# Kernel optimization log

Measured on AMD Instinct MI355X. Metric: run time of the kernel, lower is better.

Reference implementation:

```python
import jax, jax.numpy as jnp
import numpy as np


def gcn_conv(x, edge_index, W, b):
    # PyG GCNConv: h = x @ W; add self-loops; symmetric D^-1/2 (A+I) D^-1/2 aggregation; + bias
    n = x.shape[0]
    h = x @ W  # [N, out]
    loop = jnp.arange(n, dtype=edge_index.dtype)
    src = jnp.concatenate([edge_index[0], loop])  # message sources
    dst = jnp.concatenate([edge_index[1], loop])  # message targets
    ones = jnp.ones(dst.shape[0], dtype=h.dtype)
    deg = jax.ops.segment_sum(ones, dst, num_segments=n)  # in-degree incl. self-loop
    dinv = jnp.where(deg > 0, jax.lax.rsqrt(deg), 0.0)
    norm = dinv[src] * dinv[dst]  # [E+N]
    msg = h[src] * norm[:, None]  # gather + scale
    out = jax.ops.segment_sum(msg, dst, num_segments=n)  # scatter-add
    return out + b


def setup_inputs() -> dict:
    key = jax.random.key(0)
    ks = jax.random.split(key, 6)
    N, E, D = 100000, 600000, 128
    x = jax.random.normal(ks[0], (N, D), dtype=jnp.float32)
    edge_index = jax.random.randint(ks[1], (2, E), 0, N, dtype=jnp.int64)
    s = 1.0 / np.sqrt(D)
    W1 = jax.random.normal(ks[2], (D, D), dtype=jnp.float32) * s
    b1 = jnp.zeros((D,), dtype=jnp.float32)
    W2 = jax.random.normal(ks[3], (2 * D, D), dtype=jnp.float32) * (1.0 / np.sqrt(2 * D))
    b2 = jnp.zeros((D,), dtype=jnp.float32)
    Wout = jax.random.normal(ks[4], (D, 1), dtype=jnp.float32) * s
    bout = jnp.zeros((1,), dtype=jnp.float32)
    return {"x": x, "edge_index": edge_index, "W1": W1, "b1": b1,
            "W2": W2, "b2": b2, "Wout": Wout, "bout": bout}


def reference(x, edge_index, W1, b1, W2, b2, Wout, bout):
    y = gcn_conv(x, edge_index, W1, b1)          # [N, D]
    y = jnp.concatenate([x, y], axis=-1)          # [N, 2D]
    y = jax.nn.leaky_relu(y, negative_slope=0.01)
    z = gcn_conv(y, edge_index, W2, b2)           # [N, D]
    z = jax.nn.leaky_relu(z, negative_slope=0.01)
    return z @ Wout + bout                        # [N, 1]
```

## Files before the change

kernel.cpp:

```cpp
#include <hip/hip_runtime.h>

#define DIM 128
#define CAP 48

typedef _Float16 half8 __attribute__((ext_vector_type(8)));
typedef float f32x4 __attribute__((ext_vector_type(4)));

__device__ __forceinline__ float lrelu(float v) { return v > 0.f ? v : 0.01f * v; }


__global__ __launch_bounds__(256) void k_zero(int* __restrict__ cursor, int n) {
    int i = blockIdx.x * 256 + threadIdx.x;
    if (i < n) cursor[i] = 0;
}

__global__ __launch_bounds__(256) void k_fill(const int* __restrict__ src,
                                              const int* __restrict__ dst,
                                              int* __restrict__ cursor,
                                              int* __restrict__ srcs, int e) {
    int i = blockIdx.x * 256 + threadIdx.x;
    if (i >= e) return;
    int d = dst[i];
    int p = atomicAdd(&cursor[d], 1);
    if (p < CAP) srcs[(size_t)d * CAP + p] = src[i];
}

__global__ __launch_bounds__(256) void k_dinv(const int* __restrict__ cursor,
                                              float* __restrict__ dinv, int n) {
    int i = blockIdx.x * 256 + threadIdx.x;
    if (i < n) dinv[i] = rsqrtf((float)cursor[i] + 1.0f);
}

__global__ __launch_bounds__(256) void k_pack(const float* __restrict__ W,
                                              _Float16* __restrict__ Wp, int kdim) {
    int tid = blockIdx.x * 256 + threadIdx.x;
    if (tid >= kdim * 128) return;
    int jj = tid & 7;
    int frag = tid >> 3;
    int l = frag & 63;
    int cb = (frag >> 6) & 7;
    int kb = frag >> 9;
    int k = kb * 32 + ((l >> 4) << 3) + jj;
    int nn = cb * 16 + (l & 15);
    Wp[tid] = (_Float16)W[(size_t)k * DIM + nn];
}

__global__ __launch_bounds__(256, 2) void k_mm1(
    const float* __restrict__ x, const _Float16* __restrict__ Wp1,
    const _Float16* __restrict__ Wp2, const float* __restrict__ dinv,
    _Float16* __restrict__ hs, _Float16* __restrict__ P, int n) {
    __shared__ _Float16 As[8 * 4 * 64 * 8];
    const int tid = threadIdx.x;
    const int w = tid >> 6, l = tid & 63;
    const int row0 = blockIdx.x * 128;
    {
        const int c8 = (tid & 15) * 8;
        const int kb = c8 >> 5, sub = (c8 & 31) >> 3;
#pragma unroll
        for (int it = 0; it < 8; ++it) {
            int r = it * 16 + (tid >> 4);
            int grow = row0 + r;
            float4 v0 = make_float4(0.f, 0.f, 0.f, 0.f), v1 = v0;
            if (grow < n) {
                const float4* xr = (const float4*)&x[(size_t)grow * DIM + c8];
                v0 = xr[0]; v1 = xr[1];
            }
            half8 o;
            o[0] = (_Float16)v0.x; o[1] = (_Float16)v0.y;
            o[2] = (_Float16)v0.z; o[3] = (_Float16)v0.w;
            o[4] = (_Float16)v1.x; o[5] = (_Float16)v1.y;
            o[6] = (_Float16)v1.z; o[7] = (_Float16)v1.w;
            int rb = r >> 4;
            int li = sub * 16 + (r & 15);
            int p = li ^ (kb << 2);
            *(half8*)&As[(((rb << 2) + kb) * 64 + p) * 8] = o;
        }
    }
    __syncthreads();

    f32x4 ah[4][4], ap[4][4];
#pragma unroll
    for (int i = 0; i < 4; ++i)
#pragma unroll
        for (int j = 0; j < 4; ++j) {
            f32x4 z = {0.f, 0.f, 0.f, 0.f};
            ah[i][j] = z; ap[i][j] = z;
        }

    const int rwb = (w >> 1) * 4, cwb = (w & 1) * 4;
#pragma unroll
    for (int kb = 0; kb < 4; ++kb) {
        half8 a[4], al[4], b[4];
#pragma unroll
        for (int i = 0; i < 4; ++i)
            a[i] = *(const half8*)&As[((((rwb + i) << 2) + kb) * 64 + (l ^ (kb << 2))) * 8];
#pragma unroll
        for (int i = 0; i < 4; ++i)
#pragma unroll
            for (int e = 0; e < 8; ++e) {
                _Float16 t = a[i][e];
                al[i][e] = (t > (_Float16)0.f) ? t : t * (_Float16)0.01f;
            }
#pragma unroll
        for (int j = 0; j < 4; ++j)
            b[j] = *(const half8*)&Wp1[((kb * 8 + cwb + j) * 64 + l) * 8];
#pragma unroll
        for (int i = 0; i < 4; ++i)
#pragma unroll
            for (int j = 0; j < 4; ++j)
                ah[i][j] = __builtin_amdgcn_mfma_f32_16x16x32_f16(a[i], b[j], ah[i][j], 0, 0, 0);
#pragma unroll
        for (int j = 0; j < 4; ++j)
            b[j] = *(const half8*)&Wp2[((kb * 8 + cwb + j) * 64 + l) * 8];
#pragma unroll
        for (int i = 0; i < 4; ++i)
#pragma unroll
            for (int j = 0; j < 4; ++j)
                ap[i][j] = __builtin_amdgcn_mfma_f32_16x16x32_f16(al[i], b[j], ap[i][j], 0, 0, 0);
    }
#pragma unroll
    for (int i = 0; i < 4; ++i) {
        int rbase = (rwb + i) * 16 + ((l >> 4) << 2);
#pragma unroll
        for (int reg = 0; reg < 4; ++reg) {
            int grow = row0 + rbase + reg;
            if (grow < n) {
                float d = dinv[grow];
#pragma unroll
                for (int j = 0; j < 4; ++j) {
                    int col = (cwb + j) * 16 + (l & 15);
                    hs[(size_t)grow * DIM + col] = (_Float16)(ah[i][j][reg] * d);
                }
            }
        }
    }
    _Float16* pl = P + ((size_t)(blockIdx.x * 4 + w) * 64 + l) * 64;
#pragma unroll
    for (int c = 0; c < 8; ++c) {
        int q0 = 2 * c, q1 = 2 * c + 1;
        half8 o;
#pragma unroll
        for (int e = 0; e < 4; ++e) {
            o[e]     = (_Float16)ap[q0 >> 2][q0 & 3][e];
            o[4 + e] = (_Float16)ap[q1 >> 2][q1 & 3][e];
        }
        *(half8*)&pl[c * 8] = o;
    }
}

__global__ __launch_bounds__(256) void k_mm2(
    const _Float16* __restrict__ A2, const _Float16* __restrict__ Wp2,
    const _Float16* __restrict__ P, const float* __restrict__ dinv,
    _Float16* __restrict__ hs2, int n) {
    __shared__ _Float16 As[8 * 4 * 64 * 8];
    const int tid = threadIdx.x;
    const int w = tid >> 6, l = tid & 63;
    const int row0 = blockIdx.x * 128;
    const _Float16* at = A2 + (size_t)blockIdx.x * 16384;
#pragma unroll
    for (int it = 0; it < 8; ++it) {
        int idx = it * 256 + tid;
        *(half8*)&As[idx * 8] = *(const half8*)&at[(size_t)idx * 8];
    }
    __syncthreads();

    f32x4 acc[4][4];
#pragma unroll
    for (int i = 0; i < 4; ++i)
#pragma unroll
        for (int j = 0; j < 4; ++j) { f32x4 z = {0.f, 0.f, 0.f, 0.f}; acc[i][j] = z; }

    const int rwb = (w >> 1) * 4, cwb = (w & 1) * 4;
#pragma unroll
    for (int kb = 0; kb < 4; ++kb) {
        half8 a[4], b[4];
#pragma unroll
        for (int i = 0; i < 4; ++i)
            a[i] = *(const half8*)&As[((((rwb + i) << 2) + kb) * 64 + l) * 8];
#pragma unroll
        for (int j = 0; j < 4; ++j)
            b[j] = *(const half8*)&Wp2[(((kb + 4) * 8 + cwb + j) * 64 + l) * 8];
#pragma unroll
        for (int i = 0; i < 4; ++i)
#pragma unroll
            for (int j = 0; j < 4; ++j)
                acc[i][j] = __builtin_amdgcn_mfma_f32_16x16x32_f16(a[i], b[j], acc[i][j], 0, 0, 0);
    }
    const _Float16* pl = P + ((size_t)(blockIdx.x * 4 + w) * 64 + l) * 64;
#pragma unroll
    for (int c = 0; c < 8; ++c) {
        half8 pv = *(const half8*)&pl[c * 8];
        int q0 = 2 * c, q1 = 2 * c + 1;
#pragma unroll
        for (int e = 0; e < 4; ++e) {
            acc[q0 >> 2][q0 & 3][e] += (float)pv[e];
            acc[q1 >> 2][q1 & 3][e] += (float)pv[4 + e];
        }
    }
#pragma unroll
    for (int i = 0; i < 4; ++i) {
        int rbase = (rwb + i) * 16 + ((l >> 4) << 2);
#pragma unroll
        for (int reg = 0; reg < 4; ++reg) {
            int grow = row0 + rbase + reg;
            if (grow < n) {
                float d = dinv[grow];
#pragma unroll
                for (int j = 0; j < 4; ++j) {
                    int col = (cwb + j) * 16 + (l & 15);
                    hs2[(size_t)grow * DIM + col] = (_Float16)(acc[i][j][reg] * d);
                }
            }
        }
    }
}

__global__ __launch_bounds__(256) void k_gather1(
    const _Float16* __restrict__ hs, const int* __restrict__ cursor,
    const int* __restrict__ srcs, const float* __restrict__ dinv,
    const float* __restrict__ b1, _Float16* __restrict__ A2, int n) {
    const int node = blockIdx.x * 16 + (threadIdx.x >> 4);
    const int g = threadIdx.x & 15;
    if (node >= n) return;
    int cnt = cursor[node];
    if (cnt > CAP) cnt = CAP;
    const int* sl = &srcs[(size_t)node * CAP];
    half8 h = *(const half8*)&hs[(size_t)node * DIM + g * 8];
    float acc[8];
#pragma unroll
    for (int e = 0; e < 8; ++e) acc[e] = (float)h[e];
    for (int base = 0; base < cnt; base += 16) {
        int m = cnt - base;
        if (m > 16) m = 16;
        int sid = (g < m) ? sl[base + g] : 0;
#pragma unroll 4
        for (int j = 0; j < m; ++j) {
            int s = __shfl(sid, j, 16);
            half8 v = *(const half8*)&hs[(size_t)s * DIM + g * 8];
#pragma unroll
            for (int e = 0; e < 8; ++e) acc[e] += (float)v[e];
        }
    }
    const float d = dinv[node];
    const float4 bb0 = *(const float4*)&b1[g * 8];
    const float4 bb1 = *(const float4*)&b1[g * 8 + 4];
    half8 o;
    o[0] = (_Float16)lrelu(fmaf(acc[0], d, bb0.x));
    o[1] = (_Float16)lrelu(fmaf(acc[1], d, bb0.y));
    o[2] = (_Float16)lrelu(fmaf(acc[2], d, bb0.z));
    o[3] = (_Float16)lrelu(fmaf(acc[3], d, bb0.w));
    o[4] = (_Float16)lrelu(fmaf(acc[4], d, bb1.x));
    o[5] = (_Float16)lrelu(fmaf(acc[5], d, bb1.y));
    o[6] = (_Float16)lrelu(fmaf(acc[6], d, bb1.z));
    o[7] = (_Float16)lrelu(fmaf(acc[7], d, bb1.w));
    int tile = node >> 7, rb = (node >> 4) & 7, rr = node & 15;
    int kb = g >> 2, sub = g & 3;
    *(half8*)&A2[(size_t)tile * 16384 + ((((rb << 2) + kb) * 64) + sub * 16 + rr) * 8] = o;
}

__global__ __launch_bounds__(256) void k_gather2(
    const _Float16* __restrict__ hs2, const int* __restrict__ cursor,
    const int* __restrict__ srcs, const float* __restrict__ dinv,
    const float* __restrict__ b2, const float* __restrict__ wout,
    const float* __restrict__ bout, float* __restrict__ out, int n) {
    const int node = blockIdx.x * 16 + (threadIdx.x >> 4);
    const int g = threadIdx.x & 15;
    if (node >= n) return;
    int cnt = cursor[node];
    if (cnt > CAP) cnt = CAP;
    const int* sl = &srcs[(size_t)node * CAP];
    half8 h = *(const half8*)&hs2[(size_t)node * DIM + g * 8];
    float acc[8];
#pragma unroll
    for (int e = 0; e < 8; ++e) acc[e] = (float)h[e];
    for (int base = 0; base < cnt; base += 16) {
        int m = cnt - base;
        if (m > 16) m = 16;
        int sid = (g < m) ? sl[base + g] : 0;
#pragma unroll 4
        for (int j = 0; j < m; ++j) {
            int s = __shfl(sid, j, 16);
            half8 v = *(const half8*)&hs2[(size_t)s * DIM + g * 8];
#pragma unroll
            for (int e = 0; e < 8; ++e) acc[e] += (float)v[e];
        }
    }
    const float d = dinv[node];
    const float4 bb0 = *(const float4*)&b2[g * 8];
    const float4 bb1 = *(const float4*)&b2[g * 8 + 4];
    const float4 wv0 = *(const float4*)&wout[g * 8];
    const float4 wv1 = *(const float4*)&wout[g * 8 + 4];
    float s = lrelu(fmaf(acc[0], d, bb0.x)) * wv0.x + lrelu(fmaf(acc[1], d, bb0.y)) * wv0.y +
              lrelu(fmaf(acc[2], d, bb0.z)) * wv0.z + lrelu(fmaf(acc[3], d, bb0.w)) * wv0.w +
              lrelu(fmaf(acc[4], d, bb1.x)) * wv1.x + lrelu(fmaf(acc[5], d, bb1.y)) * wv1.y +
              lrelu(fmaf(acc[6], d, bb1.z)) * wv1.z + lrelu(fmaf(acc[7], d, bb1.w)) * wv1.w;
#pragma unroll
    for (int off = 8; off > 0; off >>= 1) s += __shfl_down(s, off, 16);
    if (g == 0) out[node] = s + bout[0];
}

extern "C" void kernel_launch(void* const* d_in, const int* in_sizes, int n_in,
                              void* d_out, int out_size, void* d_ws, size_t ws_size,
                              hipStream_t stream) {
    const float* x    = (const float*)d_in[0];
    const int*   ei   = (const int*)d_in[1];
    const float* W1   = (const float*)d_in[2];
    const float* b1   = (const float*)d_in[3];
    const float* W2   = (const float*)d_in[4];
    const float* b2   = (const float*)d_in[5];
    const float* Wout = (const float*)d_in[6];
    const float* bout = (const float*)d_in[7];
    float* out = (float*)d_out;

    const int N = in_sizes[0] / DIM;
    const int E = in_sizes[1] / 2;
    const int* src = ei;
    const int* dst = ei + E;

    const int gb = (N + 127) / 128;
    const size_t tileH = (size_t)gb * 16384;

    size_t Na = ((size_t)N + 63) & ~(size_t)63;
    int* cursor   = (int*)d_ws;
    float* dinv   = (float*)(cursor + Na);
    int* srcs     = (int*)(dinv + Na);
    _Float16* Wp1 = (_Float16*)(srcs + (size_t)N * CAP);
    _Float16* Wp2 = Wp1 + 128 * 128;
    _Float16* hsb = Wp2 + 256 * 128;
    _Float16* Pb  = hsb + tileH;
    _Float16* A2b = Pb + tileH;

    const int nb = (N + 255) / 256;
    const int eb = (E + 255) / 256;
    const int ab = (N + 15) / 16;

    k_zero<<<nb, 256, 0, stream>>>(cursor, N);
    k_fill<<<eb, 256, 0, stream>>>(src, dst, cursor, srcs, E);
    k_dinv<<<nb, 256, 0, stream>>>(cursor, dinv, N);
    k_pack<<<(128 * 128 + 255) / 256, 256, 0, stream>>>(W1, Wp1, 128);
    k_pack<<<(256 * 128 + 255) / 256, 256, 0, stream>>>(W2, Wp2, 256);

    k_mm1<<<gb, 256, 0, stream>>>(x, Wp1, Wp2, dinv, hsb, Pb, N);
    k_gather1<<<ab, 256, 0, stream>>>(hsb, cursor, srcs, dinv, b1, A2b, N);
    k_mm2<<<gb, 256, 0, stream>>>(A2b, Wp2, Pb, dinv, hsb, N);
    k_gather2<<<ab, 256, 0, stream>>>(hsb, cursor, srcs, dinv, b2, Wout, bout, out, N);
}
```

Before: 246.5 us.

## Fuse layer-1 gather into second GEMM and merge preprocessing kernels

Folds the first-layer neighbour aggregation into the second GEMM kernel, so the aggregated tile goes straight into shared memory and the A2 intermediate buffer is no longer written to or read from global memory. Edge fill and both weight-packing passes are merged into one kernel, and the zeroing kernel becomes a memset. The degree-normalisation array is gone; rsqrt is recomputed from the cursor counts wherever it is needed. GEMM tiles shrink to 64 rows, and the first GEMM loads A fragments directly from global memory with no LDS staging. The second-layer output is written in place over the P buffer, which saves workspace but depends on each block reading its own P tile before overwriting it.

Result: faster. 234.3 us (-4.9%).

```diff
diff --git a/kernel.cpp b/kernel.cpp
--- a/kernel.cpp
+++ b/kernel.cpp
@@ -8,271 +8,211 @@
 
 __device__ __forceinline__ float lrelu(float v) { return v > 0.f ? v : 0.01f * v; }
 
-
-__global__ __launch_bounds__(256) void k_zero(int* __restrict__ cursor, int n) {
-    int i = blockIdx.x * 256 + threadIdx.x;
-    if (i < n) cursor[i] = 0;
-}
-
-__global__ __launch_bounds__(256) void k_fill(const int* __restrict__ src,
-                                              const int* __restrict__ dst,
-                                              int* __restrict__ cursor,
-                                              int* __restrict__ srcs, int e) {
-    int i = blockIdx.x * 256 + threadIdx.x;
-    if (i >= e) return;
-    int d = dst[i];
-    int p = atomicAdd(&cursor[d], 1);
-    if (p < CAP) srcs[(size_t)d * CAP + p] = src[i];
-}
-
-__global__ __launch_bounds__(256) void k_dinv(const int* __restrict__ cursor,
-                                              float* __restrict__ dinv, int n) {
-    int i = blockIdx.x * 256 + threadIdx.x;
-    if (i < n) dinv[i] = rsqrtf((float)cursor[i] + 1.0f);
-}
-
-__global__ __launch_bounds__(256) void k_pack(const float* __restrict__ W,
-                                              _Float16* __restrict__ Wp, int kdim) {
-    int tid = blockIdx.x * 256 + threadIdx.x;
-    if (tid >= kdim * 128) return;
-    int jj = tid & 7;
-    int frag = tid >> 3;
+__global__ __launch_bounds__(256) void k_prep(
+    const int* __restrict__ src, const int* __restrict__ dst,
+    int* __restrict__ cursor, int* __restrict__ srcs, int e, int eb,
+    const float* __restrict__ W1, _Float16* __restrict__ Wp1,
+    const float* __restrict__ W2, _Float16* __restrict__ Wp2) {
+    int b = blockIdx.x;
+    if (b < eb) {
+        int i = b * 256 + threadIdx.x;
+        if (i < e) {
+            int d = dst[i];
+            int p = atomicAdd(&cursor[d], 1);
+            if (p < CAP) srcs[(size_t)d * CAP + p] = src[i];
+        }
+        return;
+    }
+    b -= eb;
+    const float* W;
+    _Float16* Wp;
+    int tid2;
+    if (b < 64) { W = W1; Wp = Wp1; tid2 = b * 256 + threadIdx.x; }
+    else        { W = W2; Wp = Wp2; tid2 = (b - 64) * 256 + threadIdx.x; }
+    int jj = tid2 & 7;
+    int frag = tid2 >> 3;
     int l = frag & 63;
     int cb = (frag >> 6) & 7;
     int kb = frag >> 9;
     int k = kb * 32 + ((l >> 4) << 3) + jj;
     int nn = cb * 16 + (l & 15);
-    Wp[tid] = (_Float16)W[(size_t)k * DIM + nn];
+    Wp[tid2] = (_Float16)W[(size_t)k * DIM + nn];
 }
 
 __global__ __launch_bounds__(256, 2) void k_mm1(
     const float* __restrict__ x, const _Float16* __restrict__ Wp1,
-    const _Float16* __restrict__ Wp2, const float* __restrict__ dinv,
+    const _Float16* __restrict__ Wp2, const int* __restrict__ cursor,
     _Float16* __restrict__ hs, _Float16* __restrict__ P, int n) {
-    __shared__ _Float16 As[8 * 4 * 64 * 8];
     const int tid = threadIdx.x;
     const int w = tid >> 6, l = tid & 63;
-    const int row0 = blockIdx.x * 128;
-    {
-        const int c8 = (tid & 15) * 8;
-        const int kb = c8 >> 5, sub = (c8 & 31) >> 3;
-#pragma unroll
-        for (int it = 0; it < 8; ++it) {
-            int r = it * 16 + (tid >> 4);
-            int grow = row0 + r;
-            float4 v0 = make_float4(0.f, 0.f, 0.f, 0.f), v1 = v0;
-            if (grow < n) {
-                const float4* xr = (const float4*)&x[(size_t)grow * DIM + c8];
-                v0 = xr[0]; v1 = xr[1];
-            }
-            half8 o;
-            o[0] = (_Float16)v0.x; o[1] = (_Float16)v0.y;
-            o[2] = (_Float16)v0.z; o[3] = (_Float16)v0.w;
-            o[4] = (_Float16)v1.x; o[5] = (_Float16)v1.y;
-            o[6] = (_Float16)v1.z; o[7] = (_Float16)v1.w;
-            int rb = r >> 4;
-            int li = sub * 16 + (r & 15);
-            int p = li ^ (kb << 2);
-            *(half8*)&As[(((rb << 2) + kb) * 64 + p) * 8] = o;
-        }
-    }
-    __syncthreads();
-
-    f32x4 ah[4][4], ap[4][4];
-#pragma unroll
-    for (int i = 0; i < 4; ++i)
-#pragma unroll
-        for (int j = 0; j < 4; ++j) {
-            f32x4 z = {0.f, 0.f, 0.f, 0.f};
-            ah[i][j] = z; ap[i][j] = z;
-        }
-
-    const int rwb = (w >> 1) * 4, cwb = (w & 1) * 4;
+    const int row0 = blockIdx.x * 64;
+    const int arow = row0 + w * 16 + (l & 15);
+    const int kq = (l >> 4) << 3;
+    const bool ok = arow < n;
+    const float* xr = &x[(size_t)arow * DIM + kq];
+
+    f32x4 ah[8], ap[8];
+#pragma unroll
+    for (int cb = 0; cb < 8; ++cb) {
+        f32x4 z = {0.f, 0.f, 0.f, 0.f};
+        ah[cb] = z; ap[cb] = z;
+    }
+
 #pragma unroll
     for (int kb = 0; kb < 4; ++kb) {
-        half8 a[4], al[4], b[4];
-#pragma unroll
-        for (int i = 0; i < 4; ++i)
-            a[i] = *(const half8*)&As[((((rwb + i) << 2) + kb) * 64 + (l ^ (kb << 2))) * 8];
-#pragma unroll
-        for (int i = 0; i < 4; ++i)
-#pragma unroll
-            for (int e = 0; e < 8; ++e) {
-                _Float16 t = a[i][e];
-                al[i][e] = (t > (_Float16)0.f) ? t : t * (_Float16)0.01f;
-            }
-#pragma unroll
-        for (int j = 0; j < 4; ++j)
-            b[j] = *(const half8*)&Wp1[((kb * 8 + cwb + j) * 64 + l) * 8];
-#pragma unroll
-        for (int i = 0; i < 4; ++i)
-#pragma unroll
-            for (int j = 0; j < 4; ++j)
-                ah[i][j] = __builtin_amdgcn_mfma_f32_16x16x32_f16(a[i], b[j], ah[i][j], 0, 0, 0);
-#pragma unroll
-        for (int j = 0; j < 4; ++j)
-            b[j] = *(const half8*)&Wp2[((kb * 8 + cwb + j) * 64 + l) * 8];
-#pragma unroll
-        for (int i = 0; i < 4; ++i)
-#pragma unroll
-            for (int j = 0; j < 4; ++j)
-                ap[i][j] = __builtin_amdgcn_mfma_f32_16x16x32_f16(al[i], b[j], ap[i][j], 0, 0, 0);
-    }
-#pragma unroll
-    for (int i = 0; i < 4; ++i) {
-        int rbase = (rwb + i) * 16 + ((l >> 4) << 2);
-#pragma unroll
-        for (int reg = 0; reg < 4; ++reg) {
-            int grow = row0 + rbase + reg;
-            if (grow < n) {
-                float d = dinv[grow];
-#pragma unroll
-                for (int j = 0; j < 4; ++j) {
-                    int col = (cwb + j) * 16 + (l & 15);
-                    hs[(size_t)grow * DIM + col] = (_Float16)(ah[i][j][reg] * d);
+        float4 v0 = make_float4(0.f, 0.f, 0.f, 0.f), v1 = v0;
+        if (ok) {
+            v0 = *(const float4*)&xr[kb * 32];
+            v1 = *(const float4*)&xr[kb * 32 + 4];
+        }
+        half8 a, al;
+        a[0] = (_Float16)v0.x; a[1] = (_Float16)v0.y;
+        a[2] = (_Float16)v0.z; a[3] = (_Float16)v0.w;
+        a[4] = (_Float16)v1.x; a[5] = (_Float16)v1.y;
+        a[6] = (_Float16)v1.z; a[7] = (_Float16)v1.w;
+#pragma unroll
+        for (int e = 0; e < 8; ++e) {
+            _Float16 t = a[e];
+            al[e] = (t > (_Float16)0.f) ? t : t * (_Float16)0.01f;
+        }
+#pragma unroll
+        for (int cb = 0; cb < 8; ++cb) {
+            half8 bf = *(const half8*)&Wp1[((kb * 8 + cb) * 64 + l) * 8];
+            ah[cb] = __builtin_amdgcn_mfma_f32_16x16x32_f16(a, bf, ah[cb], 0, 0, 0);
+        }
+#pragma unroll
+        for (int cb = 0; cb < 8; ++cb) {
+            half8 bf = *(const half8*)&Wp2[((kb * 8 + cb) * 64 + l) * 8];
+            ap[cb] = __builtin_amdgcn_mfma_f32_16x16x32_f16(al, bf, ap[cb], 0, 0, 0);
+        }
+    }
+    const int orow0 = row0 + w * 16 + ((l >> 4) << 2);
+    const int oc = l & 15;
+#pragma unroll
+    for (int reg = 0; reg < 4; ++reg) {
+        int grow = orow0 + reg;
+        if (grow < n) {
+            float d = rsqrtf((float)cursor[grow] + 1.0f);
+#pragma unroll
+            for (int cb = 0; cb < 8; ++cb)
+                hs[(size_t)grow * DIM + cb * 16 + oc] = (_Float16)(ah[cb][reg] * d);
+        }
+    }
+    _Float16* pl = P + ((size_t)(blockIdx.x * 4 + w) * 64 + l) * 32;
+#pragma unroll
+    for (int c = 0; c < 4; ++c) {
+        half8 o;
+#pragma unroll
+        for (int e = 0; e < 4; ++e) {
+            o[e]     = (_Float16)ap[2 * c][e];
+            o[4 + e] = (_Float16)ap[2 * c + 1][e];
+        }
+        *(half8*)&pl[c * 8] = o;
+    }
+}
+
+__global__ __launch_bounds__(256, 2) void k_mm2g(
+    const _Float16* __restrict__ hs, const int* __restrict__ cursor,
+    const int* __restrict__ srcs, const float* __restrict__ b1,
+    const _Float16* __restrict__ Wp2, const _Float16* __restrict__ P,
+    _Float16* __restrict__ hs2, int n) {
+    __shared__ _Float16 Af[16 * 64 * 8];
+    const int tid = threadIdx.x;
+    const int w = tid >> 6, l = tid & 63;
+    const int row0 = blockIdx.x * 64;
+
+    f32x4 acc[8];
+    const _Float16* pl = P + ((size_t)(blockIdx.x * 4 + w) * 64 + l) * 32;
+#pragma unroll
+    for (int c = 0; c < 4; ++c) {
+        half8 pv = *(const half8*)&pl[c * 8];
+#pragma unroll
+        for (int e = 0; e < 4; ++e) {
+            acc[2 * c][e]     = (float)pv[e];
+            acc[2 * c + 1][e] = (float)pv[4 + e];
+        }
+    }
+
+    const int g = tid & 15;
+#pragma unroll
+    for (int it = 0; it < 4; ++it) {
+        int node = row0 + it * 16 + (tid >> 4);
+        half8 o = 0;
+        if (node < n) {
+            int rawc = cursor[node];
+            float d = rsqrtf((float)rawc + 1.0f);
+            int cnt = rawc > CAP ? CAP : rawc;
+            const int* sl = &srcs[(size_t)node * CAP];
+            half8 h = *(const half8*)&hs[(size_t)node * DIM + g * 8];
+            float a[8];
+#pragma unroll
+            for (int e = 0; e < 8; ++e) a[e] = (float)h[e];
+            for (int base = 0; base < cnt; base += 16) {
+                int m = cnt - base;
+                if (m > 16) m = 16;
+                int sid = (g < m) ? sl[base + g] : 0;
+#pragma unroll 4
+                for (int j = 0; j < m; ++j) {
+                    int s = __shfl(sid, j, 16);
+                    half8 v = *(const half8*)&hs[(size_t)s * DIM + g * 8];
+#pragma unroll
+                    for (int e = 0; e < 8; ++e) a[e] += (float)v[e];
                 }
             }
-        }
-    }
-    _Float16* pl = P + ((size_t)(blockIdx.x * 4 + w) * 64 + l) * 64;
-#pragma unroll
-    for (int c = 0; c < 8; ++c) {
-        int q0 = 2 * c, q1 = 2 * c + 1;
-        half8 o;
-#pragma unroll
-        for (int e = 0; e < 4; ++e) {
-            o[e]     = (_Float16)ap[q0 >> 2][q0 & 3][e];
-            o[4 + e] = (_Float16)ap[q1 >> 2][q1 & 3][e];
-        }
-        *(half8*)&pl[c * 8] = o;
-    }
-}
-
-__global__ __launch_bounds__(256) void k_mm2(
-    const _Float16* __restrict__ A2, const _Float16* __restrict__ Wp2,
-    const _Float16* __restrict__ P, const float* __restrict__ dinv,
-    _Float16* __restrict__ hs2, int n) {
-    __shared__ _Float16 As[8 * 4 * 64 * 8];
-    const int tid = threadIdx.x;
-    const int w = tid >> 6, l = tid & 63;
-    const int row0 = blockIdx.x * 128;
-    const _Float16* at = A2 + (size_t)blockIdx.x * 16384;
-#pragma unroll
-    for (int it = 0; it < 8; ++it) {
-        int idx = it * 256 + tid;
-        *(half8*)&As[idx * 8] = *(const half8*)&at[(size_t)idx * 8];
+            const float4 bb0 = *(const float4*)&b1[g * 8];
+            const float4 bb1 = *(const float4*)&b1[g * 8 + 4];
+            o[0] = (_Float16)lrelu(fmaf(a[0], d, bb0.x));
+            o[1] = (_Float16)lrelu(fmaf(a[1], d, bb0.y));
+            o[2] = (_Float16)lrelu(fmaf(a[2], d, bb0.z));
+            o[3] = (_Float16)lrelu(fmaf(a[3], d, bb0.w));
+            o[4] = (_Float16)lrelu(fmaf(a[4], d, bb1.x));
+            o[5] = (_Float16)lrelu(fmaf(a[5], d, bb1.y));
+            o[6] = (_Float16)lrelu(fmaf(a[6], d, bb1.z));
+            o[7] = (_Float16)lrelu(fmaf(a[7], d, bb1.w));
+        }
+        *(half8*)&Af[(((it * 4 + (g >> 2)) * 64) + (g & 3) * 16 + (tid >> 4)) * 8] = o;
     }
     __syncthreads();
 
-    f32x4 acc[4][4];
-#pragma unroll
-    for (int i = 0; i < 4; ++i)
-#pragma unroll
-        for (int j = 0; j < 4; ++j) { f32x4 z = {0.f, 0.f, 0.f, 0.f}; acc[i][j] = z; }
-
-    const int rwb = (w >> 1) * 4, cwb = (w & 1) * 4;
 #pragma unroll
     for (int kb = 0; kb < 4; ++kb) {
-        half8 a[4], b[4];
-#pragma unroll
-        for (int i = 0; i < 4; ++i)
-            a[i] = *(const half8*)&As[((((rwb + i) << 2) + kb) * 64 + l) * 8];
-#pragma unroll
-        for (int j = 0; j < 4; ++j)
-            b[j] = *(const half8*)&Wp2[(((kb + 4) * 8 + cwb + j) * 64 + l) * 8];
-#pragma unroll
-        for (int i = 0; i < 4; ++i)
-#pragma unroll
-            for (int j = 0; j < 4; ++j)
-                acc[i][j] = __builtin_amdgcn_mfma_f32_16x16x32_f16(a[i], b[j], acc[i][j], 0, 0, 0);
-    }
-    const _Float16* pl = P + ((size_t)(blockIdx.x * 4 + w) * 64 + l) * 64;
-#pragma unroll
-    for (int c = 0; c < 8; ++c) {
-        half8 pv = *(const half8*)&pl[c * 8];
-        int q0 = 2 * c, q1 = 2 * c + 1;
-#pragma unroll
-        for (int e = 0; e < 4; ++e) {
-            acc[q0 >> 2][q0 & 3][e] += (float)pv[e];
-            acc[q1 >> 2][q1 & 3][e] += (float)pv[4 + e];
-        }
-    }
-#pragma unroll
-    for (int i = 0; i < 4; ++i) {
-        int rbase = (rwb + i) * 16 + ((l >> 4) << 2);
-#pragma unroll
-        for (int reg = 0; reg < 4; ++reg) {
-            int grow = row0 + rbase + reg;
-            if (grow < n) {
-                float d = dinv[grow];
-#pragma unroll
-                for (int j = 0; j < 4; ++j) {
-                    int col = (cwb + j) * 16 + (l & 15);
-                    hs2[(size_t)grow * DIM + col] = (_Float16)(acc[i][j][reg] * d);
-                }
-            }
-        }
-    }
-}
-
-__global__ __launch_bounds__(256) void k_gather1(
-    const _Float16* __restrict__ hs, const int* __restrict__ cursor,
-    const int* __restrict__ srcs, const float* __restrict__ dinv,
-    const float* __restrict__ b1, _Float16* __restrict__ A2, int n) {
+        half8 a = *(const half8*)&Af[((w * 4 + kb) * 64 + l) * 8];
+#pragma unroll
+        for (int cb = 0; cb < 8; ++cb) {
+            half8 bf = *(const half8*)&Wp2[(((kb + 4) * 8 + cb) * 64 + l) * 8];
+            acc[cb] = __builtin_amdgcn_mfma_f32_16x16x32_f16(a, bf, acc[cb], 0, 0, 0);
+        }
+    }
+    const int orow0 = row0 + w * 16 + ((l >> 4) << 2);
+    const int oc = l & 15;
+#pragma unroll
+    for (int reg = 0; reg < 4; ++reg) {
+        int grow = orow0 + reg;
+        if (grow < n) {
+            float d = rsqrtf((float)cursor[grow] + 1.0f);
+#pragma unroll
+            for (int cb = 0; cb < 8; ++cb)
+                hs2[(size_t)grow * DIM + cb * 16 + oc] = (_Float16)(acc[cb][reg] * d);
+        }
+    }
+}
+
+__global__ __launch_bounds__(256) void k_gather2(
+    const _Float16* __restrict__ hs2, const int* __restrict__ cursor,
+    const int* __restrict__ srcs, const float* __restrict__ b2,
+    const float* __restrict__ wout, const float* __restrict__ bout,
+    float* __restrict__ out, int n) {
     const int node = blockIdx.x * 16 + (threadIdx.x >> 4);
     const int g = threadIdx.x & 15;
     if (node >= n) return;
-    int cnt = cursor[node];
-    if (cnt > CAP) cnt = CAP;
-    const int* sl = &srcs[(size_t)node * CAP];
-    half8 h = *(const half8*)&hs[(size_t)node * DIM + g * 8];
-    float acc[8];
-#pragma unroll
-    for (int e = 0; e < 8; ++e) acc[e] = (float)h[e];
-    for (int base = 0; base < cnt; base += 16) {
-        int m = cnt - base;
-        if (m > 16) m = 16;
-        int sid = (g < m) ? sl[base + g] : 0;
-#pragma unroll 4
-        for (int j = 0; j < m; ++j) {
-            int s = __shfl(sid, j, 16);
-            half8 v = *(const half8*)&hs[(size_t)s * DIM + g * 8];
-#pragma unroll
-            for (int e = 0; e < 8; ++e) acc[e] += (float)v[e];
-        }
-    }
-    const float d = dinv[node];
-    const float4 bb0 = *(const float4*)&b1[g * 8];
-    const float4 bb1 = *(const float4*)&b1[g * 8 + 4];
-    half8 o;
-    o[0] = (_Float16)lrelu(fmaf(acc[0], d, bb0.x));
-    o[1] = (_Float16)lrelu(fmaf(acc[1], d, bb0.y));
-    o[2] = (_Float16)lrelu(fmaf(acc[2], d, bb0.z));
-    o[3] = (_Float16)lrelu(fmaf(acc[3], d, bb0.w));
-    o[4] = (_Float16)lrelu(fmaf(acc[4], d, bb1.x));
-    o[5] = (_Float16)lrelu(fmaf(acc[5], d, bb1.y));
-    o[6] = (_Float16)lrelu(fmaf(acc[6], d, bb1.z));
-    o[7] = (_Float16)lrelu(fmaf(acc[7], d, bb1.w));
-    int tile = node >> 7, rb = (node >> 4) & 7, rr = node & 15;
-    int kb = g >> 2, sub = g & 3;
-    *(half8*)&A2[(size_t)tile * 16384 + ((((rb << 2) + kb) * 64) + sub * 16 + rr) * 8] = o;
-}
-
-__global__ __launch_bounds__(256) void k_gather2(
-    const _Float16* __restrict__ hs2, const int* __restrict__ cursor,
-    const int* __restrict__ srcs, const float* __restrict__ dinv,
-    const float* __restrict__ b2, const float* __restrict__ wout,
-    const float* __restrict__ bout, float* __restrict__ out, int n) {
-    const int node = blockIdx.x * 16 + (threadIdx.x >> 4);
-    const int g = threadIdx.x & 15;
-    if (node >= n) return;
-    int cnt = cursor[node];
-    if (cnt > CAP) cnt = CAP;
+    int rawc = cursor[node];
+    float d = rsqrtf((float)rawc + 1.0f);
+    int cnt = rawc > CAP ? CAP : rawc;
     const int* sl = &srcs[(size_t)node * CAP];
     half8 h = *(const half8*)&hs2[(size_t)node * DIM + g * 8];
-    float acc[8];
-#pragma unroll
-    for (int e = 0; e < 8; ++e) acc[e] = (float)h[e];
+    float a[8];
+#pragma unroll
+    for (int e = 0; e < 8; ++e) a[e] = (float)h[e];
     for (int base = 0; base < cnt; base += 16) {
         int m = cnt - base;
         if (m > 16) m = 16;
@@ -282,18 +222,17 @@
             int s = __shfl(sid, j, 16);
             half8 v = *(const half8*)&hs2[(size_t)s * DIM + g * 8];
 #pragma unroll
-            for (int e = 0; e < 8; ++e) acc[e] += (float)v[e];
-        }
-    }
-    const float d = dinv[node];
+            for (int e = 0; e < 8; ++e) a[e] += (float)v[e];
+        }
+    }
     const float4 bb0 = *(const float4*)&b2[g * 8];
     const float4 bb1 = *(const float4*)&b2[g * 8 + 4];
     const float4 wv0 = *(const float4*)&wout[g * 8];
     const float4 wv1 = *(const float4*)&wout[g * 8 + 4];
-    float s = lrelu(fmaf(acc[0], d, bb0.x)) * wv0.x + lrelu(fmaf(acc[1], d, bb0.y)) * wv0.y +
-              lrelu(fmaf(acc[2], d, bb0.z)) * wv0.z + lrelu(fmaf(acc[3], d, bb0.w)) * wv0.w +
-              lrelu(fmaf(acc[4], d, bb1.x)) * wv1.x + lrelu(fmaf(acc[5], d, bb1.y)) * wv1.y +
-              lrelu(fmaf(acc[6], d, bb1.z)) * wv1.z + lrelu(fmaf(acc[7], d, bb1.w)) * wv1.w;
+    float s = lrelu(fmaf(a[0], d, bb0.x)) * wv0.x + lrelu(fmaf(a[1], d, bb0.y)) * wv0.y +
+              lrelu(fmaf(a[2], d, bb0.z)) * wv0.z + lrelu(fmaf(a[3], d, bb0.w)) * wv0.w +
+              lrelu(fmaf(a[4], d, bb1.x)) * wv1.x + lrelu(fmaf(a[5], d, bb1.y)) * wv1.y +
+              lrelu(fmaf(a[6], d, bb1.z)) * wv1.z + lrelu(fmaf(a[7], d, bb1.w)) * wv1.w;
 #pragma unroll
     for (int off = 8; off > 0; off >>= 1) s += __shfl_down(s, off, 16);
     if (g == 0) out[node] = s + bout[0];
@@ -317,31 +256,22 @@
     const int* src = ei;
     const int* dst = ei + E;
 
-    const int gb = (N + 127) / 128;
-    const size_t tileH = (size_t)gb * 16384;
+    const int gb = (N + 63) / 64;
 
     size_t Na = ((size_t)N + 63) & ~(size_t)63;
     int* cursor   = (int*)d_ws;
-    float* dinv   = (float*)(cursor + Na);
-    int* srcs     = (int*)(dinv + Na);
+    int* srcs     = cursor + Na;
     _Float16* Wp1 = (_Float16*)(srcs + (size_t)N * CAP);
     _Float16* Wp2 = Wp1 + 128 * 128;
     _Float16* hsb = Wp2 + 256 * 128;
-    _Float16* Pb  = hsb + tileH;
-    _Float16* A2b = Pb + tileH;
-
-    const int nb = (N + 255) / 256;
+    _Float16* Pb  = hsb + (size_t)N * DIM;
+
     const int eb = (E + 255) / 256;
     const int ab = (N + 15) / 16;
 
-    k_zero<<<nb, 256, 0, stream>>>(cursor, N);
-    k_fill<<<eb, 256, 0, stream>>>(src, dst, cursor, srcs, E);
-    k_dinv<<<nb, 256, 0, stream>>>(cursor, dinv, N);
-    k_pack<<<(128 * 128 + 255) / 256, 256, 0, stream>>>(W1, Wp1, 128);
-    k_pack<<<(256 * 128 + 255) / 256, 256, 0, stream>>>(W2, Wp2, 256);
-
-    k_mm1<<<gb, 256, 0, stream>>>(x, Wp1, Wp2, dinv, hsb, Pb, N);
-    k_gather1<<<ab, 256, 0, stream>>>(hsb, cursor, srcs, dinv, b1, A2b, N);
-    k_mm2<<<gb, 256, 0, stream>>>(A2b, Wp2, Pb, dinv, hsb, N);
-    k_gather2<<<ab, 256, 0, stream>>>(hsb, cursor, srcs, dinv, b2, Wout, bout, out, N);
-}
+    hipMemsetAsync(cursor, 0, (size_t)N * sizeof(int), stream);
+    k_prep<<<eb + 64 + 128, 256, 0, stream>>>(src, dst, cursor, srcs, E, eb, W1, Wp1, W2, Wp2);
+    k_mm1<<<gb, 256, 0, stream>>>(x, Wp1, Wp2, cursor, hsb, Pb, N);
+    k_mm2g<<<gb, 256, 0, stream>>>(hsb, cursor, srcs, b1, Wp2, Pb, Pb, N);
+    k_gather2<<<ab, 256, 0, stream>>>(Pb, cursor, srcs, b2, Wout, bout, out, N);
+}
```
